# Kernel tuning notes

Hardware: AMD Instinct MI355X
Metric: run time of the kernel (lower is better)

The kernel has to match this reference:

```python
import jax, jax.numpy as jnp
import numpy as np

T, B, D_G, D_H, D_OUT = 16, 64, 512, 1024, 512
S = 3            # inner fast-weight refinement steps
LAM = 0.95       # lambda_decay
ETA = 0.5
EPS = 1e-6       # cfg.epsilon
LN_EPS = 1e-5    # torch LayerNorm default


def setup_inputs() -> dict:
    key = jax.random.key(0)
    ks = jax.random.split(key, 8)
    z_seq = jax.random.normal(ks[0], (T, B, D_G), dtype=jnp.float32)
    clean_vec = jax.random.normal(ks[1], (B, D_OUT), dtype=jnp.float32)
    # kaiming_uniform_ for W_h (relu), xavier for W_g -- uniform approximations
    bh_w = float(np.sqrt(6.0 / D_H))
    W_h = jax.random.uniform(ks[2], (D_H, D_H), jnp.float32, -bh_w, bh_w)
    bg_w = float(np.sqrt(6.0 / (D_G + D_H)))
    W_g = jax.random.uniform(ks[3], (D_H, D_G), jnp.float32, -bg_w, bg_w)
    b_h = jnp.zeros((D_H,), jnp.float32)
    ln_gamma = jnp.ones((D_H,), jnp.float32)
    ln_beta = jnp.zeros((D_H,), jnp.float32)
    alpha_fw = jnp.asarray(1.0, jnp.float32)
    hw = float(np.sqrt(6.0 / (D_H + D_OUT)))
    head_W = jax.random.uniform(ks[4], (D_OUT, D_H), jnp.float32, -hw, hw)
    head_b = jnp.zeros((D_OUT,), jnp.float32)
    return {"z_seq": z_seq, "clean_vec": clean_vec, "W_h": W_h, "W_g": W_g,
            "b_h": b_h, "ln_gamma": ln_gamma, "ln_beta": ln_beta,
            "alpha_fw": alpha_fw, "head_W": head_W, "head_b": head_b}


def _ln(x, g, b):
    mu = jnp.mean(x, axis=-1, keepdims=True)
    var = jnp.mean((x - mu) ** 2, axis=-1, keepdims=True)
    return (x - mu) * jax.lax.rsqrt(var + LN_EPS) * g + b


def _compute_k(alpha):
    k_pos = 1.0 + jax.nn.softplus(alpha)
    k_neg = 1.0 / (1.0 + jax.nn.softplus(-alpha))
    return jnp.where(alpha >= 0, k_pos, k_neg)


def reference(z_seq, clean_vec, W_h, W_g, b_h, ln_gamma, ln_beta, alpha_fw, head_W, head_b):
    k = _compute_k(alpha_fw)

    def step(carry, z_t):
        h, A = carry
        h_base = h @ W_h.T + z_t @ W_g.T + b_h           # [B, d_h]
        h = jax.nn.relu(_ln(h_base, ln_gamma, ln_beta))
        for _ in range(S):
            Ah = jnp.einsum('bij,bj->bi', A, h)           # fast-weight read
            dot = jnp.sum(h * Ah, axis=1, keepdims=True)
            n1 = jnp.linalg.norm(h, axis=1, keepdims=True) + 1e-6
            n2 = jnp.linalg.norm(Ah, axis=1, keepdims=True) + 1e-6
            R = dot / (n1 * n2 + 1e-6)
            R_pos = jnp.clip(R, 0.0, 1.0)
            a_dyn = 1.0 - (1.0 - R_pos) ** k
            h = (1.0 - a_dyn ** 2) * h_base + a_dyn * Ah
            h = jax.nn.relu(_ln(h, ln_gamma, ln_beta))
        # Hebbian outer-product update
        A = LAM * A + ETA * jnp.einsum('bi,bj->bij', h, h)
        return (h, A), None

    h0 = jnp.zeros((B, D_H), z_seq.dtype)
    A0 = jnp.zeros((B, D_H, D_H), z_seq.dtype)
    (h, A), _ = jax.lax.scan(step, (h0, A0), z_seq[:-1])

    # last timestep: plain refinement, no gating, no A update
    z_T = z_seq[-1]
    h_base = h @ W_h.T + z_T @ W_g.T + b_h
    h = jax.nn.relu(_ln(h_base, ln_gamma, ln_beta))
    for _ in range(S):
        Ah = jnp.einsum('bij,bj->bi', A, h)
        h = jax.nn.relu(_ln(h_base + Ah, ln_gamma, ln_beta))

    pred_vec = h @ head_W.T + head_b
    pred_norm = pred_vec / (jnp.linalg.norm(pred_vec, axis=1, keepdims=True) + 1e-6)
    clean_norm = clean_vec / (jnp.linalg.norm(clean_vec, axis=1, keepdims=True) + 1e-6)
    diff = pred_vec - clean_vec
    sq_err = jnp.sum(diff ** 2, axis=1)
    denom = jnp.sum(clean_vec ** 2, axis=1) + EPS
    loss = jnp.mean(sq_err / denom)
    acc = jnp.mean(jnp.sum(pred_norm * clean_norm, axis=1))
    return loss, acc
```

## Files before the change

### kernel.cpp

```cpp
#include <hip/hip_runtime.h>

#define D_G   512
#define D_H   1024
#define D_OUT 512
#define BATCH 64
#define LAMv  0.95f
#define ETAv  0.5f


__device__ inline float4 f4fma(float4 w, float s, float4 a) {
  a.x = fmaf(w.x, s, a.x); a.y = fmaf(w.y, s, a.y);
  a.z = fmaf(w.z, s, a.z); a.w = fmaf(w.w, s, a.w);
  return a;
}

__global__ __launch_bounds__(256) void k_tr3(const float* __restrict__ Wh,
                                             const float* __restrict__ Wg,
                                             const float* __restrict__ hW,
                                             float* __restrict__ WhT,
                                             float* __restrict__ WgT,
                                             float* __restrict__ hWT) {
  __shared__ float t[64][65];
  const int id = blockIdx.x;
  const float* src; float* dst; int R, C, bx, by;
  if (id < 256)      { src = Wh; dst = WhT; R = 1024; C = 1024;
                       bx = id & 15;        by = id >> 4; }
  else if (id < 384) { src = Wg; dst = WgT; R = 1024; C = 512;
                       bx = (id-256) & 7;   by = (id-256) >> 3; }
  else               { src = hW; dst = hWT; R = 512;  C = 1024;
                       bx = (id-384) & 15;  by = (id-384) >> 4; }
  const int c0 = bx * 64, r0 = by * 64;
  const int tid = threadIdx.x;
  const int lr = tid >> 4;
  const int lc = (tid & 15) * 4;
#pragma unroll
  for (int p = 0; p < 4; ++p) {
    int r = lr + p * 16;
    float4 v = *(const float4*)&src[(size_t)(r0 + r) * C + c0 + lc];
    t[r][lc] = v.x; t[r][lc+1] = v.y; t[r][lc+2] = v.z; t[r][lc+3] = v.w;
  }
  __syncthreads();
#pragma unroll
  for (int p = 0; p < 4; ++p) {
    int c = lr + p * 16;
    float4 v = make_float4(t[lc][c], t[lc+1][c], t[lc+2][c], t[lc+3][c]);
    *(float4*)&dst[(size_t)(c0 + c) * R + r0 + lc] = v;
  }
}

__global__ __launch_bounds__(256) void k_zg(const float* __restrict__ z,
                                            const float* __restrict__ WgT,
                                            const float* __restrict__ bh,
                                            float* __restrict__ zg) {
  const int lane = threadIdx.x & 63;
  const int wid  = __builtin_amdgcn_readfirstlane(threadIdx.x >> 6);
  const int iq   = blockIdx.x * 64 + lane;
  const int b0   = blockIdx.y * 8 + wid * 2;
  const int t    = blockIdx.z;
  const float4* w4  = (const float4*)WgT;
  const float4* zr0 = (const float4*)(z + ((size_t)t * BATCH + b0) * D_G);
  const float4* zr1 = (const float4*)(z + ((size_t)t * BATCH + b0 + 1) * D_G);
  float4 A0 = {0,0,0,0}, A1 = {0,0,0,0};
#pragma unroll 2
  for (int jq = 0; jq < D_G / 4; ++jq) {
    float4 zv0 = zr0[jq], zv1 = zr1[jq];
    float4 wa = w4[(size_t)jq*1024 +       iq];
    float4 wb = w4[(size_t)jq*1024 + 256 + iq];
    float4 wc = w4[(size_t)jq*1024 + 512 + iq];
    float4 wd = w4[(size_t)jq*1024 + 768 + iq];
    A0 = f4fma(wa, zv0.x, A0); A0 = f4fma(wb, zv0.y, A0);
    A0 = f4fma(wc, zv0.z, A0); A0 = f4fma(wd, zv0.w, A0);
    A1 = f4fma(wa, zv1.x, A1); A1 = f4fma(wb, zv1.y, A1);
    A1 = f4fma(wc, zv1.z, A1); A1 = f4fma(wd, zv1.w, A1);
  }
  float4 bias = ((const float4*)bh)[iq];
  A0.x += bias.x; A0.y += bias.y; A0.z += bias.z; A0.w += bias.w;
  A1.x += bias.x; A1.y += bias.y; A1.z += bias.z; A1.w += bias.w;
  float4* o = (float4*)(zg + (size_t)t * (BATCH * D_H));
  o[(size_t)b0 * 256 + iq] = A0;
  o[(size_t)(b0 + 1) * 256 + iq] = A1;
}

__global__ __launch_bounds__(256) void k_hbase(const float* __restrict__ hprev,
                                               const float* __restrict__ WhT,
                                               float* __restrict__ outp) {
  const int lane = threadIdx.x & 63;
  const int wid  = __builtin_amdgcn_readfirstlane(threadIdx.x >> 6);
  const int iq   = blockIdx.x * 64 + lane;
  const int b0   = blockIdx.y * 8 + wid * 2;
  const int k    = blockIdx.z;
  const float4* w4  = (const float4*)WhT;
  const float4* h0  = (const float4*)(hprev + (size_t)b0 * D_H);
  const float4* h1  = (const float4*)(hprev + (size_t)(b0 + 1) * D_H);
  float4 A0 = {0,0,0,0}, A1 = {0,0,0,0};
  const int jq0 = k * 16;
#pragma unroll 2
  for (int jq = jq0; jq < jq0 + 16; ++jq) {
    float4 hv0 = h0[jq], hv1 = h1[jq];
    float4 wa = w4[(size_t)jq*1024 +       iq];
    float4 wb = w4[(size_t)jq*1024 + 256 + iq];
    float4 wc = w4[(size_t)jq*1024 + 512 + iq];
    float4 wd = w4[(size_t)jq*1024 + 768 + iq];
    A0 = f4fma(wa, hv0.x, A0); A0 = f4fma(wb, hv0.y, A0);
    A0 = f4fma(wc, hv0.z, A0); A0 = f4fma(wd, hv0.w, A0);
    A1 = f4fma(wa, hv1.x, A1); A1 = f4fma(wb, hv1.y, A1);
    A1 = f4fma(wc, hv1.z, A1); A1 = f4fma(wd, hv1.w, A1);
  }
  float4* o = (float4*)(outp + (size_t)k * (BATCH * D_H));
  o[(size_t)b0 * 256 + iq] = A0;
  o[(size_t)(b0 + 1) * 256 + iq] = A1;
}

__device__ inline float wred(float x) {
#pragma unroll
  for (int off = 32; off > 0; off >>= 1) x += __shfl_down(x, off);
  return x;
}

template<int T>
__global__ __launch_bounds__(256) void k_refine(
    const float* __restrict__ hbp, const float* __restrict__ zg,
    float* __restrict__ hist,
    const float* __restrict__ gamma, const float* __restrict__ beta,
    const float* __restrict__ alphap) {
  constexpr int TS = (T > 0) ? T : 1;
  __shared__ float lh[TS][D_H];
  __shared__ float red[2][64];
  const int tid = threadIdx.x;
  const int b   = blockIdx.x;
  const int lane = tid & 63, w = tid >> 6;

  if constexpr (T > 0) {
    const float4* hist4 = (const float4*)hist;
    float4* lh4 = (float4*)lh;
#pragma unroll
    for (int s = 0; s < T; ++s)
      lh4[s * 256 + tid] = hist4[((size_t)s * BATCH + b) * 256 + tid];
  }

  float4 hb = ((const float4*)(zg + (size_t)b * D_H))[tid];
  if constexpr (T > 0) {
    const float4* p = (const float4*)hbp;
    const size_t o = (size_t)b * 256 + tid;
#pragma unroll
    for (int k = 0; k < 16; ++k) {
      float4 pk = p[o + (size_t)k * 16384];
      hb.x += pk.x; hb.y += pk.y; hb.z += pk.z; hb.w += pk.w;
    }
  }
  const float4 gi = ((const float4*)gamma)[tid];
  const float4 bi = ((const float4*)beta)[tid];
  const float al = alphap[0];
  const float kk = (al >= 0.f) ? (1.f + log1pf(expf(al)))
                               : (1.f / (1.f + log1pf(expf(-al))));

  {
    float r0 = wred((hb.x + hb.y) + (hb.z + hb.w));
    float r1 = wred((hb.x*hb.x + hb.y*hb.y) + (hb.z*hb.z + hb.w*hb.w));
    if (lane == 0) { red[0][w] = r0; red[0][4 + w] = r1; }
  }
  __syncthreads();
  const float Shb  = (red[0][0] + red[0][1]) + (red[0][2] + red[0][3]);
  const float Shb2 = (red[0][4] + red[0][5]) + (red[0][6] + red[0][7]);
  float mu  = Shb * (1.f / D_H);
  float var = Shb2 * (1.f / D_H) - mu * mu;
  float rs  = rsqrtf(var + 1e-5f);
  float4 hc;
  hc.x = fmaxf(0.f, (hb.x - mu) * rs * gi.x + bi.x);
  hc.y = fmaxf(0.f, (hb.y - mu) * rs * gi.y + bi.y);
  hc.z = fmaxf(0.f, (hb.z - mu) * rs * gi.z + bi.z);
  hc.w = fmaxf(0.f, (hb.w - mu) * rs * gi.w + bi.w);

  if constexpr (T == 0) {
    ((float4*)(hist + (size_t)b * D_H))[tid] = hc;
    return;
  } else {
    const float4* lh4 = (const float4*)lh;
#pragma unroll 1
    for (int r = 0; r < 3; ++r) {
      float pd[T];
#pragma unroll
      for (int s = 0; s < T; ++s) {
        float4 lv = lh4[s * 256 + tid];
        pd[s] = (hc.x*lv.x + hc.y*lv.y) + (hc.z*lv.z + hc.w*lv.w);
      }
#pragma unroll
      for (int s = 0; s < T; ++s) {
        float t = wred(pd[s]);
        if (lane == 0) red[1][s * 4 + w] = t;
      }
      __syncthreads();
      float cf[T];
      {
        float lamc = ETAv;
#pragma unroll
        for (int s = T - 1; s >= 0; --s) {
          float ds = (red[1][s*4] + red[1][s*4+1])
                   + (red[1][s*4+2] + red[1][s*4+3]);
          cf[s] = lamc * ds;
          lamc *= LAMv;
        }
      }
      float4 ah = {0.f, 0.f, 0.f, 0.f};
#pragma unroll
      for (int s = 0; s < T; ++s) {
        float4 lv = lh4[s * 256 + tid];
        ah.x = fmaf(cf[s], lv.x, ah.x); ah.y = fmaf(cf[s], lv.y, ah.y);
        ah.z = fmaf(cf[s], lv.z, ah.z); ah.w = fmaf(cf[s], lv.w, ah.w);
      }
      {
        float q0 = wred((hc.x*ah.x + hc.y*ah.y) + (hc.z*ah.z + hc.w*ah.w));
        float q1 = wred((hc.x*hc.x + hc.y*hc.y) + (hc.z*hc.z + hc.w*hc.w));
        float q2 = wred((ah.x*ah.x + ah.y*ah.y) + (ah.z*ah.z + ah.w*ah.w));
        float q3 = wred((hb.x*ah.x + hb.y*ah.y) + (hb.z*ah.z + hb.w*ah.w));
        float q4 = wred((ah.x + ah.y) + (ah.z + ah.w));
        if (lane == 0) {
          red[0][w] = q0; red[0][4+w] = q1; red[0][8+w] = q2;
          red[0][12+w] = q3; red[0][16+w] = q4;
        }
      }
      __syncthreads();
      float S_hAh  = (red[0][0]+red[0][1])+(red[0][2]+red[0][3]);
      float S_h2   = (red[0][4]+red[0][5])+(red[0][6]+red[0][7]);
      float S_Ah2  = (red[0][8]+red[0][9])+(red[0][10]+red[0][11]);
      float S_hbAh = (red[0][12]+red[0][13])+(red[0][14]+red[0][15]);
      float S_ah   = (red[0][16]+red[0][17])+(red[0][18]+red[0][19]);
      float n1 = sqrtf(S_h2) + 1e-6f;
      float n2 = sqrtf(S_Ah2) + 1e-6f;
      float R  = S_hAh / (n1 * n2 + 1e-6f);
      float Rp = fminf(fmaxf(R, 0.f), 1.f);
      float ad = 1.f - powf(1.f - Rp, kk);
      float oma = 1.f - ad * ad;
      float4 hn;
      hn.x = oma*hb.x + ad*ah.x; hn.y = oma*hb.y + ad*ah.y;
      hn.z = oma*hb.z + ad*ah.z; hn.w = oma*hb.w + ad*ah.w;
      float Shn  = oma * Shb + ad * S_ah;
      float Shn2 = oma*oma*Shb2 + 2.f*oma*ad*S_hbAh + ad*ad*S_Ah2;
      float mu2  = Shn * (1.f / D_H);
      float var2 = Shn2 * (1.f / D_H) - mu2 * mu2;
      float rs2  = rsqrtf(var2 + 1e-5f);
      hc.x = fmaxf(0.f, (hn.x - mu2) * rs2 * gi.x + bi.x);
      hc.y = fmaxf(0.f, (hn.y - mu2) * rs2 * gi.y + bi.y);
      hc.z = fmaxf(0.f, (hn.z - mu2) * rs2 * gi.z + bi.z);
      hc.w = fmaxf(0.f, (hn.w - mu2) * rs2 * gi.w + bi.w);
    }
    ((float4*)(hist + ((size_t)T * BATCH + b) * D_H))[tid] = hc;
  }
}

__global__ __launch_bounds__(256) void k_refine_final(
    const float* __restrict__ hbp, const float* __restrict__ zg,
    const float* __restrict__ hist, float* __restrict__ hfin,
    const float* __restrict__ gamma, const float* __restrict__ beta) {
  __shared__ float lh[15][D_H];
  __shared__ float red[2][64];
  const int tid = threadIdx.x;
  const int b   = blockIdx.x;
  const int lane = tid & 63, w = tid >> 6;
  {
    const float4* hist4 = (const float4*)hist;
    float4* lh4 = (float4*)lh;
#pragma unroll
    for (int s = 0; s < 15; ++s)
      lh4[s * 256 + tid] = hist4[((size_t)s * BATCH + b) * 256 + tid];
  }
  float4 hb = ((const float4*)(zg + (size_t)b * D_H))[tid];
  {
    const float4* p = (const float4*)hbp;
    const size_t o = (size_t)b * 256 + tid;
#pragma unroll
    for (int k = 0; k < 16; ++k) {
      float4 pk = p[o + (size_t)k * 16384];
      hb.x += pk.x; hb.y += pk.y; hb.z += pk.z; hb.w += pk.w;
    }
  }
  const float4 gi = ((const float4*)gamma)[tid];
  const float4 bi = ((const float4*)beta)[tid];

  {
    float r0 = wred((hb.x + hb.y) + (hb.z + hb.w));
    float r1 = wred((hb.x*hb.x + hb.y*hb.y) + (hb.z*hb.z + hb.w*hb.w));
    if (lane == 0) { red[0][w] = r0; red[0][4 + w] = r1; }
  }
  __syncthreads();
  const float Shb  = (red[0][0] + red[0][1]) + (red[0][2] + red[0][3]);
  const float Shb2 = (red[0][4] + red[0][5]) + (red[0][6] + red[0][7]);
  float mu  = Shb * (1.f / D_H);
  float var = Shb2 * (1.f / D_H) - mu * mu;
  float rs  = rsqrtf(var + 1e-5f);
  float4 hc;
  hc.x = fmaxf(0.f, (hb.x - mu) * rs * gi.x + bi.x);
  hc.y = fmaxf(0.f, (hb.y - mu) * rs * gi.y + bi.y);
  hc.z = fmaxf(0.f, (hb.z - mu) * rs * gi.z + bi.z);
  hc.w = fmaxf(0.f, (hb.w - mu) * rs * gi.w + bi.w);

  const float4* lh4 = (const float4*)lh;
#pragma unroll 1
  for (int r = 0; r < 3; ++r) {
    float pd[15];
#pragma unroll
    for (int s = 0; s < 15; ++s) {
      float4 lv = lh4[s * 256 + tid];
      pd[s] = (hc.x*lv.x + hc.y*lv.y) + (hc.z*lv.z + hc.w*lv.w);
    }
#pragma unroll
    for (int s = 0; s < 15; ++s) {
      float t = wred(pd[s]);
      if (lane == 0) red[1][s * 4 + w] = t;
    }
    __syncthreads();
    float cf[15];
    {
      float lamc = ETAv;
#pragma unroll
      for (int s = 14; s >= 0; --s) {
        float ds = (red[1][s*4] + red[1][s*4+1])
                 + (red[1][s*4+2] + red[1][s*4+3]);
        cf[s] = lamc * ds;
        lamc *= LAMv;
      }
    }
    float4 ah = {0.f, 0.f, 0.f, 0.f};
#pragma unroll
    for (int s = 0; s < 15; ++s) {
      float4 lv = lh4[s * 256 + tid];
      ah.x = fmaf(cf[s], lv.x, ah.x); ah.y = fmaf(cf[s], lv.y, ah.y);
      ah.z = fmaf(cf[s], lv.z, ah.z); ah.w = fmaf(cf[s], lv.w, ah.w);
    }
    {
      float q0 = wred((hb.x*ah.x + hb.y*ah.y) + (hb.z*ah.z + hb.w*ah.w));
      float q1 = wred((ah.x*ah.x + ah.y*ah.y) + (ah.z*ah.z + ah.w*ah.w));
      float q2 = wred((ah.x + ah.y) + (ah.z + ah.w));
      if (lane == 0) { red[0][w] = q0; red[0][4+w] = q1; red[0][8+w] = q2; }
    }
    __syncthreads();
    float S_hbAh = (red[0][0]+red[0][1])+(red[0][2]+red[0][3]);
    float S_Ah2  = (red[0][4]+red[0][5])+(red[0][6]+red[0][7]);
    float S_ah   = (red[0][8]+red[0][9])+(red[0][10]+red[0][11]);
    float4 hn;
    hn.x = hb.x + ah.x; hn.y = hb.y + ah.y;
    hn.z = hb.z + ah.z; hn.w = hb.w + ah.w;
    float Shn  = Shb + S_ah;
    float Shn2 = Shb2 + 2.f * S_hbAh + S_Ah2;
    float mu2  = Shn * (1.f / D_H);
    float var2 = Shn2 * (1.f / D_H) - mu2 * mu2;
    float rs2  = rsqrtf(var2 + 1e-5f);
    hc.x = fmaxf(0.f, (hn.x - mu2) * rs2 * gi.x + bi.x);
    hc.y = fmaxf(0.f, (hn.y - mu2) * rs2 * gi.y + bi.y);
    hc.z = fmaxf(0.f, (hn.z - mu2) * rs2 * gi.z + bi.z);
    hc.w = fmaxf(0.f, (hn.w - mu2) * rs2 * gi.w + bi.w);
  }
  ((float4*)(hfin + (size_t)b * D_H))[tid] = hc;
}

__global__ __launch_bounds__(256) void k_head(const float* __restrict__ hfin,
                                              const float* __restrict__ hWT,
                                              float* __restrict__ predp) {
  const int lane = threadIdx.x & 63;
  const int wid  = __builtin_amdgcn_readfirstlane(threadIdx.x >> 6);
  const int oq   = blockIdx.x * 64 + lane;
  const int b0   = blockIdx.y * 8 + wid * 2;
  const int k    = blockIdx.z;
  const float4* w4 = (const float4*)hWT;
  const float4* h0 = (const float4*)(hfin + (size_t)b0 * D_H);
  const float4* h1 = (const float4*)(hfin + (size_t)(b0 + 1) * D_H);
  float4 A0 = {0,0,0,0}, A1 = {0,0,0,0};
  const int jq0 = k * 16;
#pragma unroll 2
  for (int jq = jq0; jq < jq0 + 16; ++jq) {
    float4 hv0 = h0[jq], hv1 = h1[jq];
    float4 wa = w4[(size_t)jq*512 +       oq];
    float4 wb = w4[(size_t)jq*512 + 128 + oq];
    float4 wc = w4[(size_t)jq*512 + 256 + oq];
    float4 wd = w4[(size_t)jq*512 + 384 + oq];
    A0 = f4fma(wa, hv0.x, A0); A0 = f4fma(wb, hv0.y, A0);
    A0 = f4fma(wc, hv0.z, A0); A0 = f4fma(wd, hv0.w, A0);
    A1 = f4fma(wa, hv1.x, A1); A1 = f4fma(wb, hv1.y, A1);
    A1 = f4fma(wc, hv1.z, A1); A1 = f4fma(wd, hv1.w, A1);
  }
  float4* o = (float4*)(predp + (size_t)k * (BATCH * D_OUT));
  o[(size_t)b0 * 128 + oq] = A0;
  o[(size_t)(b0 + 1) * 128 + oq] = A1;
}

__global__ __launch_bounds__(256) void k_loss_b(
    const float* __restrict__ predp, const float* __restrict__ hbias,
    const float* __restrict__ clean, float* __restrict__ bvals) {
  __shared__ float red[16];
  const int b = blockIdx.x;
  const int tid = threadIdx.x;
  const int lane = tid & 63, w = tid >> 6;
  float sd = 0, sc = 0, spc = 0, sp = 0;
#pragma unroll
  for (int e = 0; e < 2; ++e) {
    const int o = e * 256 + tid;
    const size_t idx = (size_t)b * D_OUT + o;
    float p = hbias[o];
#pragma unroll
    for (int k = 0; k < 16; ++k) p += predp[idx + (size_t)k * 32768];
    float c = clean[idx];
    float d = p - c;
    sd = fmaf(d, d, sd); sc = fmaf(c, c, sc);
    spc = fmaf(p, c, spc); sp = fmaf(p, p, sp);
  }
  sd = wred(sd); sc = wred(sc); spc = wred(spc); sp = wred(sp);
  if (lane == 0) {
    red[w] = sd; red[4 + w] = sc; red[8 + w] = spc; red[12 + w] = sp;
  }
  __syncthreads();
  if (tid == 0) {
    float Sd  = (red[0] + red[1]) + (red[2] + red[3]);
    float Sc  = (red[4] + red[5]) + (red[6] + red[7]);
    float Spc = (red[8] + red[9]) + (red[10] + red[11]);
    float Sp  = (red[12] + red[13]) + (red[14] + red[15]);
    bvals[b * 2 + 0] = Sd / (Sc + 1e-6f);
    bvals[b * 2 + 1] = Spc / ((sqrtf(Sp) + 1e-6f) * (sqrtf(Sc) + 1e-6f));
  }
}

__global__ __launch_bounds__(64) void k_final(const float* __restrict__ bvals,
                                              float* __restrict__ out) {
  const int tid = threadIdx.x;
  float l = bvals[tid * 2 + 0];
  float a = bvals[tid * 2 + 1];
  l = wred(l); a = wred(a);
  if (tid == 0) { out[0] = l * (1.f / BATCH); out[1] = a * (1.f / BATCH); }
}

extern "C" void kernel_launch(void* const* d_in, const int* in_sizes, int n_in,
                              void* d_out, int out_size, void* d_ws, size_t ws_size,
                              hipStream_t stream) {
  (void)in_sizes; (void)n_in; (void)out_size; (void)ws_size;
  const float* z     = (const float*)d_in[0];
  const float* clean = (const float*)d_in[1];
  const float* Wh    = (const float*)d_in[2];
  const float* Wg    = (const float*)d_in[3];
  const float* bh    = (const float*)d_in[4];
  const float* gam   = (const float*)d_in[5];
  const float* bet   = (const float*)d_in[6];
  const float* alp   = (const float*)d_in[7];
  const float* hW    = (const float*)d_in[8];
  const float* hbias = (const float*)d_in[9];

  float* ws    = (float*)d_ws;
  float* hist  = ws;
  float* hbp   = hist + 15 * 65536;
  float* zg    = hbp + 16 * 65536;
  float* hfin  = zg + 16 * 65536;
  float* predp = hfin + 65536;
  float* bvals = predp + 16 * 32768;
  float* WhT   = bvals + 128;
  float* WgT   = WhT + 1024 * 1024;
  float* hWT   = WgT + 512 * 1024;

  k_tr3<<<dim3(512), dim3(256), 0, stream>>>(Wh, Wg, hW, WhT, WgT, hWT);

  k_zg<<<dim3(4, 8, 16), dim3(256), 0, stream>>>(z, WgT, bh, zg);

#define REFINE_CASE(T) case T: \
    k_refine<T><<<dim3(64), dim3(256), 0, stream>>>( \
        hbp, zg + (size_t)T * 65536, hist, gam, bet, alp); break;

  k_refine<0><<<dim3(64), dim3(256), 0, stream>>>(hbp, zg, hist, gam, bet, alp);

  for (int t = 1; t < 15; ++t) {
    k_hbase<<<dim3(4, 8, 16), dim3(256), 0, stream>>>(
        hist + (size_t)(t - 1) * 65536, WhT, hbp);
    switch (t) {
      REFINE_CASE(1)  REFINE_CASE(2)  REFINE_CASE(3)  REFINE_CASE(4)
      REFINE_CASE(5)  REFINE_CASE(6)  REFINE_CASE(7)  REFINE_CASE(8)
      REFINE_CASE(9)  REFINE_CASE(10) REFINE_CASE(11) REFINE_CASE(12)
      REFINE_CASE(13) REFINE_CASE(14)
    }
  }
#undef REFINE_CASE

  k_hbase<<<dim3(4, 8, 16), dim3(256), 0, stream>>>(
      hist + (size_t)14 * 65536, WhT, hbp);
  k_refine_final<<<dim3(64), dim3(256), 0, stream>>>(
      hbp, zg + (size_t)15 * 65536, hist, hfin, gam, bet);
  k_head<<<dim3(2, 8, 16), dim3(256), 0, stream>>>(hfin, hWT, predp);
  k_loss_b<<<dim3(64), dim3(256), 0, stream>>>(predp, hbias, clean, bvals);
  k_final<<<dim3(1), dim3(64), 0, stream>>>(bvals, (float*)d_out);
}
```

Baseline: 425.1 us.

## Fuse whole recurrence into one persistent per-batch kernel with in-block W_h matvec

Replaces the per-timestep launches of the W_h matvec and the refinement kernels with a single kernel where each block owns one batch row. The block keeps its h history in shared memory and computes the recurrent matvec itself each step. This removes about thirty launches and the partial-sum round trips through global memory. In exchange, each of the 64 blocks streams the full W_h matrix every timestep, and only 64 workgroups are active, which concentrates bandwidth demand on a few CUs.

```diff
diff --git a/kernel.cpp b/kernel.cpp
--- a/kernel.cpp
+++ b/kernel.cpp
@@ -12,6 +12,12 @@
   a.x = fmaf(w.x, s, a.x); a.y = fmaf(w.y, s, a.y);
   a.z = fmaf(w.z, s, a.z); a.w = fmaf(w.w, s, a.w);
   return a;
+}
+
+__device__ inline float wred(float x) {
+#pragma unroll
+  for (int off = 32; off > 0; off >>= 1) x += __shfl_down(x, off);
+  return x;
 }
 
 __global__ __launch_bounds__(256) void k_tr3(const float* __restrict__ Wh,
@@ -81,79 +87,138 @@
   o[(size_t)(b0 + 1) * 256 + iq] = A1;
 }
 
-__global__ __launch_bounds__(256) void k_hbase(const float* __restrict__ hprev,
-                                               const float* __restrict__ WhT,
-                                               float* __restrict__ outp) {
-  const int lane = threadIdx.x & 63;
-  const int wid  = __builtin_amdgcn_readfirstlane(threadIdx.x >> 6);
-  const int iq   = blockIdx.x * 64 + lane;
-  const int b0   = blockIdx.y * 8 + wid * 2;
-  const int k    = blockIdx.z;
-  const float4* w4  = (const float4*)WhT;
-  const float4* h0  = (const float4*)(hprev + (size_t)b0 * D_H);
-  const float4* h1  = (const float4*)(hprev + (size_t)(b0 + 1) * D_H);
-  float4 A0 = {0,0,0,0}, A1 = {0,0,0,0};
-  const int jq0 = k * 16;
-#pragma unroll 2
-  for (int jq = jq0; jq < jq0 + 16; ++jq) {
-    float4 hv0 = h0[jq], hv1 = h1[jq];
-    float4 wa = w4[(size_t)jq*1024 +       iq];
-    float4 wb = w4[(size_t)jq*1024 + 256 + iq];
-    float4 wc = w4[(size_t)jq*1024 + 512 + iq];
-    float4 wd = w4[(size_t)jq*1024 + 768 + iq];
-    A0 = f4fma(wa, hv0.x, A0); A0 = f4fma(wb, hv0.y, A0);
-    A0 = f4fma(wc, hv0.z, A0); A0 = f4fma(wd, hv0.w, A0);
-    A1 = f4fma(wa, hv1.x, A1); A1 = f4fma(wb, hv1.y, A1);
-    A1 = f4fma(wc, hv1.z, A1); A1 = f4fma(wd, hv1.w, A1);
-  }
-  float4* o = (float4*)(outp + (size_t)k * (BATCH * D_H));
-  o[(size_t)b0 * 256 + iq] = A0;
-  o[(size_t)(b0 + 1) * 256 + iq] = A1;
-}
-
-__device__ inline float wred(float x) {
-#pragma unroll
-  for (int off = 32; off > 0; off >>= 1) x += __shfl_down(x, off);
-  return x;
-}
-
-template<int T>
-__global__ __launch_bounds__(256) void k_refine(
-    const float* __restrict__ hbp, const float* __restrict__ zg,
-    float* __restrict__ hist,
+__device__ inline float4 matvec_wh(float4 hb, const float* __restrict__ hp,
+                                   const float4* __restrict__ w4, int tid) {
+#pragma unroll 1
+  for (int k = 0; k < 16; ++k) {
+    float4 P = {0.f, 0.f, 0.f, 0.f};
+    const int jq0 = k * 16;
+#pragma unroll
+    for (int jq = jq0; jq < jq0 + 16; ++jq) {
+      float4 hv = ((const float4*)hp)[jq];
+      float4 wa = w4[(size_t)jq*1024 +       tid];
+      float4 wb = w4[(size_t)jq*1024 + 256 + tid];
+      float4 wc = w4[(size_t)jq*1024 + 512 + tid];
+      float4 wd = w4[(size_t)jq*1024 + 768 + tid];
+      P = f4fma(wa, hv.x, P); P = f4fma(wb, hv.y, P);
+      P = f4fma(wc, hv.z, P); P = f4fma(wd, hv.w, P);
+    }
+    hb.x += P.x; hb.y += P.y; hb.z += P.z; hb.w += P.w;
+  }
+  return hb;
+}
+
+__global__ __launch_bounds__(256) void k_recur(
+    const float* __restrict__ zg, const float* __restrict__ WhT,
     const float* __restrict__ gamma, const float* __restrict__ beta,
-    const float* __restrict__ alphap) {
-  constexpr int TS = (T > 0) ? T : 1;
-  __shared__ float lh[TS][D_H];
+    const float* __restrict__ alphap, float* __restrict__ hfin) {
+  __shared__ float lh[15][D_H];
   __shared__ float red[2][64];
+  __shared__ float lamp[16];
   const int tid = threadIdx.x;
   const int b   = blockIdx.x;
   const int lane = tid & 63, w = tid >> 6;
-
-  if constexpr (T > 0) {
-    const float4* hist4 = (const float4*)hist;
-    float4* lh4 = (float4*)lh;
-#pragma unroll
-    for (int s = 0; s < T; ++s)
-      lh4[s * 256 + tid] = hist4[((size_t)s * BATCH + b) * 256 + tid];
-  }
-
-  float4 hb = ((const float4*)(zg + (size_t)b * D_H))[tid];
-  if constexpr (T > 0) {
-    const float4* p = (const float4*)hbp;
-    const size_t o = (size_t)b * 256 + tid;
-#pragma unroll
-    for (int k = 0; k < 16; ++k) {
-      float4 pk = p[o + (size_t)k * 16384];
-      hb.x += pk.x; hb.y += pk.y; hb.z += pk.z; hb.w += pk.w;
-    }
+  const float4* w4 = (const float4*)WhT;
+  float4* lh4 = (float4*)lh;
+
+  if (tid == 0) {
+    float v = ETAv;
+    lamp[0] = v;
+#pragma unroll
+    for (int m = 1; m < 15; ++m) { v *= LAMv; lamp[m] = v; }
   }
   const float4 gi = ((const float4*)gamma)[tid];
   const float4 bi = ((const float4*)beta)[tid];
   const float al = alphap[0];
   const float kk = (al >= 0.f) ? (1.f + log1pf(expf(al)))
                                : (1.f / (1.f + log1pf(expf(-al))));
-
+  float4 hc;
+
+#pragma unroll 1
+  for (int t = 0; t < 15; ++t) {
+    __syncthreads();
+    float4 hb = ((const float4*)zg)[((size_t)t * BATCH + b) * 256 + tid];
+    if (t > 0) hb = matvec_wh(hb, lh[t - 1], w4, tid);
+
+    {
+      float r0 = wred((hb.x + hb.y) + (hb.z + hb.w));
+      float r1 = wred((hb.x*hb.x + hb.y*hb.y) + (hb.z*hb.z + hb.w*hb.w));
+      if (lane == 0) { red[0][w] = r0; red[0][4 + w] = r1; }
+    }
+    __syncthreads();
+    const float Shb  = (red[0][0] + red[0][1]) + (red[0][2] + red[0][3]);
+    const float Shb2 = (red[0][4] + red[0][5]) + (red[0][6] + red[0][7]);
+    float mu  = Shb * (1.f / D_H);
+    float var = Shb2 * (1.f / D_H) - mu * mu;
+    float rs  = rsqrtf(var + 1e-5f);
+    hc.x = fmaxf(0.f, (hb.x - mu) * rs * gi.x + bi.x);
+    hc.y = fmaxf(0.f, (hb.y - mu) * rs * gi.y + bi.y);
+    hc.z = fmaxf(0.f, (hb.z - mu) * rs * gi.z + bi.z);
+    hc.w = fmaxf(0.f, (hb.w - mu) * rs * gi.w + bi.w);
+
+    if (t > 0) {
+#pragma unroll 1
+      for (int r = 0; r < 3; ++r) {
+        for (int s = 0; s < t; ++s) {
+          float4 lv = lh4[s * 256 + tid];
+          float p = (hc.x*lv.x + hc.y*lv.y) + (hc.z*lv.z + hc.w*lv.w);
+          p = wred(p);
+          if (lane == 0) red[1][s * 4 + w] = p;
+        }
+        __syncthreads();
+        float4 ah = {0.f, 0.f, 0.f, 0.f};
+        for (int s = 0; s < t; ++s) {
+          float ds = (red[1][s*4] + red[1][s*4+1])
+                   + (red[1][s*4+2] + red[1][s*4+3]);
+          float coef = lamp[t - 1 - s] * ds;
+          float4 lv = lh4[s * 256 + tid];
+          ah.x = fmaf(coef, lv.x, ah.x); ah.y = fmaf(coef, lv.y, ah.y);
+          ah.z = fmaf(coef, lv.z, ah.z); ah.w = fmaf(coef, lv.w, ah.w);
+        }
+        {
+          float q0 = wred((hc.x*ah.x + hc.y*ah.y) + (hc.z*ah.z + hc.w*ah.w));
+          float q1 = wred((hc.x*hc.x + hc.y*hc.y) + (hc.z*hc.z + hc.w*hc.w));
+          float q2 = wred((ah.x*ah.x + ah.y*ah.y) + (ah.z*ah.z + ah.w*ah.w));
+          float q3 = wred((hb.x*ah.x + hb.y*ah.y) + (hb.z*ah.z + hb.w*ah.w));
+          float q4 = wred((ah.x + ah.y) + (ah.z + ah.w));
+          if (lane == 0) {
+            red[0][w] = q0; red[0][4+w] = q1; red[0][8+w] = q2;
+            red[0][12+w] = q3; red[0][16+w] = q4;
+          }
+        }
+        __syncthreads();
+        float S_hAh  = (red[0][0]+red[0][1])+(red[0][2]+red[0][3]);
+        float S_h2   = (red[0][4]+red[0][5])+(red[0][6]+red[0][7]);
+        float S_Ah2  = (red[0][8]+red[0][9])+(red[0][10]+red[0][11]);
+        float S_hbAh = (red[0][12]+red[0][13])+(red[0][14]+red[0][15]);
+        float S_ah   = (red[0][16]+red[0][17])+(red[0][18]+red[0][19]);
+        float n1 = sqrtf(S_h2) + 1e-6f;
+        float n2 = sqrtf(S_Ah2) + 1e-6f;
+        float R  = S_hAh / (n1 * n2 + 1e-6f);
+        float Rp = fminf(fmaxf(R, 0.f), 1.f);
+        float ad = 1.f - powf(1.f - Rp, kk);
+        float oma = 1.f - ad * ad;
+        float4 hn;
+        hn.x = oma*hb.x + ad*ah.x; hn.y = oma*hb.y + ad*ah.y;
+        hn.z = oma*hb.z + ad*ah.z; hn.w = oma*hb.w + ad*ah.w;
+        float Shn  = oma * Shb + ad * S_ah;
+        float Shn2 = oma*oma*Shb2 + 2.f*oma*ad*S_hbAh + ad*ad*S_Ah2;
+        float mu2  = Shn * (1.f / D_H);
+        float var2 = Shn2 * (1.f / D_H) - mu2 * mu2;
+        float rs2  = rsqrtf(var2 + 1e-5f);
+        hc.x = fmaxf(0.f, (hn.x - mu2) * rs2 * gi.x + bi.x);
+        hc.y = fmaxf(0.f, (hn.y - mu2) * rs2 * gi.y + bi.y);
+        hc.z = fmaxf(0.f, (hn.z - mu2) * rs2 * gi.z + bi.z);
+        hc.w = fmaxf(0.f, (hn.w - mu2) * rs2 * gi.w + bi.w);
+        if (r < 2) __syncthreads();
+      }
+    }
+    lh4[t * 256 + tid] = hc;
+  }
+
+  __syncthreads();
+  float4 hb = ((const float4*)zg)[((size_t)15 * BATCH + b) * 256 + tid];
+  hb = matvec_wh(hb, lh[14], w4, tid);
   {
     float r0 = wred((hb.x + hb.y) + (hb.z + hb.w));
     float r1 = wred((hb.x*hb.x + hb.y*hb.y) + (hb.z*hb.z + hb.w*hb.w));
@@ -165,167 +230,27 @@
   float mu  = Shb * (1.f / D_H);
   float var = Shb2 * (1.f / D_H) - mu * mu;
   float rs  = rsqrtf(var + 1e-5f);
-  float4 hc;
   hc.x = fmaxf(0.f, (hb.x - mu) * rs * gi.x + bi.x);
   hc.y = fmaxf(0.f, (hb.y - mu) * rs * gi.y + bi.y);
   hc.z = fmaxf(0.f, (hb.z - mu) * rs * gi.z + bi.z);
   hc.w = fmaxf(0.f, (hb.w - mu) * rs * gi.w + bi.w);
-
-  if constexpr (T == 0) {
-    ((float4*)(hist + (size_t)b * D_H))[tid] = hc;
-    return;
-  } else {
-    const float4* lh4 = (const float4*)lh;
-#pragma unroll 1
-    for (int r = 0; r < 3; ++r) {
-      float pd[T];
-#pragma unroll
-      for (int s = 0; s < T; ++s) {
-        float4 lv = lh4[s * 256 + tid];
-        pd[s] = (hc.x*lv.x + hc.y*lv.y) + (hc.z*lv.z + hc.w*lv.w);
-      }
-#pragma unroll
-      for (int s = 0; s < T; ++s) {
-        float t = wred(pd[s]);
-        if (lane == 0) red[1][s * 4 + w] = t;
-      }
-      __syncthreads();
-      float cf[T];
-      {
-        float lamc = ETAv;
-#pragma unroll
-        for (int s = T - 1; s >= 0; --s) {
-          float ds = (red[1][s*4] + red[1][s*4+1])
-                   + (red[1][s*4+2] + red[1][s*4+3]);
-          cf[s] = lamc * ds;
-          lamc *= LAMv;
-        }
-      }
-      float4 ah = {0.f, 0.f, 0.f, 0.f};
-#pragma unroll
-      for (int s = 0; s < T; ++s) {
-        float4 lv = lh4[s * 256 + tid];
-        ah.x = fmaf(cf[s], lv.x, ah.x); ah.y = fmaf(cf[s], lv.y, ah.y);
-        ah.z = fmaf(cf[s], lv.z, ah.z); ah.w = fmaf(cf[s], lv.w, ah.w);
-      }
-      {
-        float q0 = wred((hc.x*ah.x + hc.y*ah.y) + (hc.z*ah.z + hc.w*ah.w));
-        float q1 = wred((hc.x*hc.x + hc.y*hc.y) + (hc.z*hc.z + hc.w*hc.w));
-        float q2 = wred((ah.x*ah.x + ah.y*ah.y) + (ah.z*ah.z + ah.w*ah.w));
-        float q3 = wred((hb.x*ah.x + hb.y*ah.y) + (hb.z*ah.z + hb.w*ah.w));
-        float q4 = wred((ah.x + ah.y) + (ah.z + ah.w));
-        if (lane == 0) {
-          red[0][w] = q0; red[0][4+w] = q1; red[0][8+w] = q2;
-          red[0][12+w] = q3; red[0][16+w] = q4;
-        }
-      }
-      __syncthreads();
-      float S_hAh  = (red[0][0]+red[0][1])+(red[0][2]+red[0][3]);
-      float S_h2   = (red[0][4]+red[0][5])+(red[0][6]+red[0][7]);
-      float S_Ah2  = (red[0][8]+red[0][9])+(red[0][10]+red[0][11]);
-      float S_hbAh = (red[0][12]+red[0][13])+(red[0][14]+red[0][15]);
-      float S_ah   = (red[0][16]+red[0][17])+(red[0][18]+red[0][19]);
-      float n1 = sqrtf(S_h2) + 1e-6f;
-      float n2 = sqrtf(S_Ah2) + 1e-6f;
-      float R  = S_hAh / (n1 * n2 + 1e-6f);
-      float Rp = fminf(fmaxf(R, 0.f), 1.f);
-      float ad = 1.f - powf(1.f - Rp, kk);
-      float oma = 1.f - ad * ad;
-      float4 hn;
-      hn.x = oma*hb.x + ad*ah.x; hn.y = oma*hb.y + ad*ah.y;
-      hn.z = oma*hb.z + ad*ah.z; hn.w = oma*hb.w + ad*ah.w;
-      float Shn  = oma * Shb + ad * S_ah;
-      float Shn2 = oma*oma*Shb2 + 2.f*oma*ad*S_hbAh + ad*ad*S_Ah2;
-      float mu2  = Shn * (1.f / D_H);
-      float var2 = Shn2 * (1.f / D_H) - mu2 * mu2;
-      float rs2  = rsqrtf(var2 + 1e-5f);
-      hc.x = fmaxf(0.f, (hn.x - mu2) * rs2 * gi.x + bi.x);
-      hc.y = fmaxf(0.f, (hn.y - mu2) * rs2 * gi.y + bi.y);
-      hc.z = fmaxf(0.f, (hn.z - mu2) * rs2 * gi.z + bi.z);
-      hc.w = fmaxf(0.f, (hn.w - mu2) * rs2 * gi.w + bi.w);
-    }
-    ((float4*)(hist + ((size_t)T * BATCH + b) * D_H))[tid] = hc;
-  }
-}
-
-__global__ __launch_bounds__(256) void k_refine_final(
-    const float* __restrict__ hbp, const float* __restrict__ zg,
-    const float* __restrict__ hist, float* __restrict__ hfin,
-    const float* __restrict__ gamma, const float* __restrict__ beta) {
-  __shared__ float lh[15][D_H];
-  __shared__ float red[2][64];
-  const int tid = threadIdx.x;
-  const int b   = blockIdx.x;
-  const int lane = tid & 63, w = tid >> 6;
-  {
-    const float4* hist4 = (const float4*)hist;
-    float4* lh4 = (float4*)lh;
-#pragma unroll
-    for (int s = 0; s < 15; ++s)
-      lh4[s * 256 + tid] = hist4[((size_t)s * BATCH + b) * 256 + tid];
-  }
-  float4 hb = ((const float4*)(zg + (size_t)b * D_H))[tid];
-  {
-    const float4* p = (const float4*)hbp;
-    const size_t o = (size_t)b * 256 + tid;
-#pragma unroll
-    for (int k = 0; k < 16; ++k) {
-      float4 pk = p[o + (size_t)k * 16384];
-      hb.x += pk.x; hb.y += pk.y; hb.z += pk.z; hb.w += pk.w;
-    }
-  }
-  const float4 gi = ((const float4*)gamma)[tid];
-  const float4 bi = ((const float4*)beta)[tid];
-
-  {
-    float r0 = wred((hb.x + hb.y) + (hb.z + hb.w));
-    float r1 = wred((hb.x*hb.x + hb.y*hb.y) + (hb.z*hb.z + hb.w*hb.w));
-    if (lane == 0) { red[0][w] = r0; red[0][4 + w] = r1; }
-  }
-  __syncthreads();
-  const float Shb  = (red[0][0] + red[0][1]) + (red[0][2] + red[0][3]);
-  const float Shb2 = (red[0][4] + red[0][5]) + (red[0][6] + red[0][7]);
-  float mu  = Shb * (1.f / D_H);
-  float var = Shb2 * (1.f / D_H) - mu * mu;
-  float rs  = rsqrtf(var + 1e-5f);
-  float4 hc;
-  hc.x = fmaxf(0.f, (hb.x - mu) * rs * gi.x + bi.x);
-  hc.y = fmaxf(0.f, (hb.y - mu) * rs * gi.y + bi.y);
-  hc.z = fmaxf(0.f, (hb.z - mu) * rs * gi.z + bi.z);
-  hc.w = fmaxf(0.f, (hb.w - mu) * rs * gi.w + bi.w);
-
-  const float4* lh4 = (const float4*)lh;
 #pragma unroll 1
   for (int r = 0; r < 3; ++r) {
-    float pd[15];
-#pragma unroll
     for (int s = 0; s < 15; ++s) {
       float4 lv = lh4[s * 256 + tid];
-      pd[s] = (hc.x*lv.x + hc.y*lv.y) + (hc.z*lv.z + hc.w*lv.w);
-    }
-#pragma unroll
+      float p = (hc.x*lv.x + hc.y*lv.y) + (hc.z*lv.z + hc.w*lv.w);
+      p = wred(p);
+      if (lane == 0) red[1][s * 4 + w] = p;
+    }
+    __syncthreads();
+    float4 ah = {0.f, 0.f, 0.f, 0.f};
     for (int s = 0; s < 15; ++s) {
-      float t = wred(pd[s]);
-      if (lane == 0) red[1][s * 4 + w] = t;
-    }
-    __syncthreads();
-    float cf[15];
-    {
-      float lamc = ETAv;
-#pragma unroll
-      for (int s = 14; s >= 0; --s) {
-        float ds = (red[1][s*4] + red[1][s*4+1])
-                 + (red[1][s*4+2] + red[1][s*4+3]);
-        cf[s] = lamc * ds;
-        lamc *= LAMv;
-      }
-    }
-    float4 ah = {0.f, 0.f, 0.f, 0.f};
-#pragma unroll
-    for (int s = 0; s < 15; ++s) {
+      float ds = (red[1][s*4] + red[1][s*4+1])
+               + (red[1][s*4+2] + red[1][s*4+3]);
+      float coef = lamp[14 - s] * ds;
       float4 lv = lh4[s * 256 + tid];
-      ah.x = fmaf(cf[s], lv.x, ah.x); ah.y = fmaf(cf[s], lv.y, ah.y);
-      ah.z = fmaf(cf[s], lv.z, ah.z); ah.w = fmaf(cf[s], lv.w, ah.w);
+      ah.x = fmaf(coef, lv.x, ah.x); ah.y = fmaf(coef, lv.y, ah.y);
+      ah.z = fmaf(coef, lv.z, ah.z); ah.w = fmaf(coef, lv.w, ah.w);
     }
     {
       float q0 = wred((hb.x*ah.x + hb.y*ah.y) + (hb.z*ah.z + hb.w*ah.w));
@@ -349,6 +274,7 @@
     hc.y = fmaxf(0.f, (hn.y - mu2) * rs2 * gi.y + bi.y);
     hc.z = fmaxf(0.f, (hn.z - mu2) * rs2 * gi.z + bi.z);
     hc.w = fmaxf(0.f, (hn.w - mu2) * rs2 * gi.w + bi.w);
+    if (r < 2) __syncthreads();
   }
   ((float4*)(hfin + (size_t)b * D_H))[tid] = hc;
 }
@@ -443,9 +369,7 @@
   const float* hbias = (const float*)d_in[9];
 
   float* ws    = (float*)d_ws;
-  float* hist  = ws;
-  float* hbp   = hist + 15 * 65536;
-  float* zg    = hbp + 16 * 65536;
+  float* zg    = ws;
   float* hfin  = zg + 16 * 65536;
   float* predp = hfin + 65536;
   float* bvals = predp + 16 * 32768;
@@ -454,31 +378,8 @@
   float* hWT   = WgT + 512 * 1024;
 
   k_tr3<<<dim3(512), dim3(256), 0, stream>>>(Wh, Wg, hW, WhT, WgT, hWT);
-
   k_zg<<<dim3(4, 8, 16), dim3(256), 0, stream>>>(z, WgT, bh, zg);
-
-#define REFINE_CASE(T) case T: \
-    k_refine<T><<<dim3(64), dim3(256), 0, stream>>>( \
-        hbp, zg + (size_t)T * 65536, hist, gam, bet, alp); break;
-
-  k_refine<0><<<dim3(64), dim3(256), 0, stream>>>(hbp, zg, hist, gam, bet, alp);
-
-  for (int t = 1; t < 15; ++t) {
-    k_hbase<<<dim3(4, 8, 16), dim3(256), 0, stream>>>(
-        hist + (size_t)(t - 1) * 65536, WhT, hbp);
-    switch (t) {
-      REFINE_CASE(1)  REFINE_CASE(2)  REFINE_CASE(3)  REFINE_CASE(4)
-      REFINE_CASE(5)  REFINE_CASE(6)  REFINE_CASE(7)  REFINE_CASE(8)
-      REFINE_CASE(9)  REFINE_CASE(10) REFINE_CASE(11) REFINE_CASE(12)
-      REFINE_CASE(13) REFINE_CASE(14)
-    }
-  }
-#undef REFINE_CASE
-
-  k_hbase<<<dim3(4, 8, 16), dim3(256), 0, stream>>>(
-      hist + (size_t)14 * 65536, WhT, hbp);
-  k_refine_final<<<dim3(64), dim3(256), 0, stream>>>(
-      hbp, zg + (size_t)15 * 65536, hist, hfin, gam, bet);
+  k_recur<<<dim3(64), dim3(256), 0, stream>>>(zg, WhT, gam, bet, alp, hfin);
   k_head<<<dim3(2, 8, 16), dim3(256), 0, stream>>>(hfin, hWT, predp);
   k_loss_b<<<dim3(64), dim3(256), 0, stream>>>(predp, hbias, clean, bvals);
   k_final<<<dim3(1), dim3(64), 0, stream>>>(bvals, (float*)d_out);
```

New measurement: 1.069 ms. 2.51x slower.
